# Kernel optimization log

Measured on AMD Instinct MI355X. Metric: run time of the kernel, lower is better.

Reference implementation:

```python
import jax, jax.numpy as jnp
import numpy as np

# --- obs layout constants (from source) ---
OBS_TERM_DIMS = (3, 3, 3, 3, 29, 29, 29, 96)
HISTORY_LEN = 5
BASE_LIN_VEL_DIM = 3
_OFFS = [0]
for d in OBS_TERM_DIMS[:-1]:
    _OFFS.append(_OFFS[-1] + d * HISTORY_LEN)

N = 131072

def _extract_frame(x, frame_idx):
    # proprio frame: 7 terms, 99 dims total
    parts = []
    for t in range(7):
        d = OBS_TERM_DIMS[t]
        s = _OFFS[t] + frame_idx * d
        parts.append(x[:, s:s + d])
    return jnp.concatenate(parts, axis=-1)

def _extract_elevation(x):
    s = _OFFS[7] + (HISTORY_LEN - 1) * OBS_TERM_DIMS[7]
    return x[:, s:s + OBS_TERM_DIMS[7]]  # [N,96]

def setup_inputs() -> dict:
    key = jax.random.key(0)
    ks = jax.random.split(key, 16)
    s = 0.05
    return {
        "x": jax.random.normal(ks[0], (N, 975), jnp.float32),
        "vae_W1": jax.random.normal(ks[1], (480, 256), jnp.float32) * s,
        "vae_b1": jnp.zeros((256,), jnp.float32),
        "vae_Wz": jax.random.normal(ks[2], (256, 32), jnp.float32) * s,
        "vae_bz": jnp.zeros((32,), jnp.float32),
        "vae_Wv": jax.random.normal(ks[3], (256, 3), jnp.float32) * s,
        "vae_bv": jnp.zeros((3,), jnp.float32),
        "ae_W1": jax.random.normal(ks[4], (96, 64), jnp.float32) * s,
        "ae_b1": jnp.zeros((64,), jnp.float32),
        "ae_W2": jax.random.normal(ks[5], (64, 32), jnp.float32) * s,
        "ae_b2": jnp.zeros((32,), jnp.float32),
        "gate_W1": jax.random.normal(ks[6], (32, 64), jnp.float32) * s,
        "gate_b1": jnp.zeros((64,), jnp.float32),
        "gate_W2": jax.random.normal(ks[7], (64, 5), jnp.float32) * s,
        "gate_b2": jnp.zeros((5,), jnp.float32),
        "eW1": jax.random.normal(ks[8], (5, 166, 128), jnp.float32) * s,
        "eb1": jnp.zeros((5, 128), jnp.float32),
        "eW2": jax.random.normal(ks[9], (5, 128, 128), jnp.float32) * s,
        "eb2": jnp.zeros((5, 128), jnp.float32),
        "eW3": jax.random.normal(ks[10], (5, 128, 29), jnp.float32) * s,
        "eb3": jnp.zeros((5, 29), jnp.float32),
    }

def reference(x, vae_W1, vae_b1, vae_Wz, vae_bz, vae_Wv, vae_bv,
              ae_W1, ae_b1, ae_W2, ae_b2,
              gate_W1, gate_b1, gate_W2, gate_b2,
              eW1, eb1, eW2, eb2, eW3, eb3):
    elu = jax.nn.elu
    # feature extraction
    o_t = _extract_frame(x, HISTORY_LEN - 1)                       # [N,99]
    frames = [_extract_frame(x, i)[:, BASE_LIN_VEL_DIM:] for i in range(HISTORY_LEN)]
    vae_hist = jnp.concatenate(frames, axis=-1)                    # [N,480]
    e_t = _extract_elevation(x)                                    # [N,96]
    # VAE estimator (no_grad in original)
    h = elu(vae_hist @ vae_W1 + vae_b1)
    z_H = jax.lax.stop_gradient(h @ vae_Wz + vae_bz)               # [N,32]
    v_pred = jax.lax.stop_gradient(h @ vae_Wv + vae_bv)            # [N,3]
    # AE estimator (no_grad)
    ha = elu(e_t @ ae_W1 + ae_b1)
    z_E = jax.lax.stop_gradient(ha @ ae_W2 + ae_b2)                # [N,32]
    # experts: batched GEMM over 5 experts
    inp = jnp.concatenate([o_t, v_pred, z_H, z_E], axis=-1)        # [N,166]
    h1 = elu(jnp.einsum('ni,eih->neh', inp, eW1) + eb1)            # [N,5,128]
    h2 = elu(jnp.einsum('neh,ehk->nek', h1, eW2) + eb2)            # [N,5,128]
    acts = jnp.einsum('neh,ehk->nek', h2, eW3) + eb3               # [N,5,29]
    # gating
    gl = elu(z_E @ gate_W1 + gate_b1) @ gate_W2 + gate_b2          # [N,5]
    w = jax.nn.softmax(gl, axis=-1)
    return jnp.einsum('ne,nek->nk', w, acts)                       # [N,29]
```

## Files before the change

kernel.cpp:

```cpp
#include <hip/hip_runtime.h>
#include <math.h>

typedef _Float16 f16;
typedef f16  f16x8 __attribute__((ext_vector_type(8)));
typedef float f32x4 __attribute__((ext_vector_type(4)));
typedef unsigned short ushort_t;

#define MFMA16(a, b, c) __builtin_amdgcn_mfma_f32_16x16x32_f16((a), (b), (c), 0, 0, 0)

#define W1T_E 0
#define WZV_E 131072
#define A1T_E 143360
#define A2T_E 149504
#define G1T_E 151552
#define G2T_E 153600
#define E1T_E 154624
#define E2T_E 277504
#define E3T_E 359424
#define F32_B 759808

#define S2_OFF   0
#define B0_OFF   36864
#define H2_OFF   17408
#define ELEV_OFF 62528
#define HA_OFF   62528
#define ZE_OFF   71744
#define WF_OFF   75840
#define SMEM_SZ  77888

__device__ __forceinline__ float elu_f(float v) {
    float e = __expf(v) - 1.f;
    return v > 0.f ? v : e;
}

__device__ __forceinline__ unsigned pk(float a, float b) {
    ushort_t u0 = __builtin_bit_cast(ushort_t, (f16)a);
    ushort_t u1 = __builtin_bit_cast(ushort_t, (f16)b);
    return (unsigned)u0 | ((unsigned)u1 << 16);
}

__device__ __forceinline__ void store4(f16* p, f32x4 v) {
    uint2 t; t.x = pk(v[0], v[1]); t.y = pk(v[2], v[3]);
    *(uint2*)p = t;
}

__device__ __forceinline__ void elu_store4(f16* p, f32x4 v) {
    uint2 t; t.x = pk(elu_f(v[0]), elu_f(v[1])); t.y = pk(elu_f(v[2]), elu_f(v[3]));
    *(uint2*)p = t;
}

__global__ void prep_kernel(const float* __restrict__ vW1, const float* __restrict__ vWz,
                            const float* __restrict__ vWv, const float* __restrict__ aW1,
                            const float* __restrict__ aW2, const float* __restrict__ gW1,
                            const float* __restrict__ gW2, const float* __restrict__ eW1,
                            const float* __restrict__ eW2, const float* __restrict__ eW3,
                            const float* __restrict__ vbz, const float* __restrict__ vbv,
                            const float* __restrict__ eb3, const float* __restrict__ gb2,
                            char* __restrict__ ws)
{
    int i = blockIdx.x * 256 + threadIdx.x;
    f16* H = (f16*)ws;
    if (i < 131072) {
        int c = i >> 9, ks = i & 511;
        int xcol = 12 + ks;
        float v = 0.f;
        if (xcol >= 15 && xcol <= 494) {
            int hc;
            if (xcol < 60) {
                int t = xcol / 15; int rm = xcol - 15 * t; int f = rm / 3;
                hc = 96 * f + 3 * (t - 1) + (rm - 3 * f);
            } else {
                int t2 = (xcol - 60) / 145; int rm = xcol - 60 - 145 * t2; int f = rm / 29;
                hc = 96 * f + 9 + 29 * t2 + (rm - 29 * f);
            }
            v = vW1[hc * 256 + c];
        }
        H[i] = (f16)v;
    } else if (i < 143360) {
        int j = i - 131072; int c = j / 256, k = j - c * 256;
        float v = (c < 32) ? vWz[k * 32 + c] : ((c < 35) ? vWv[k * 3 + (c - 32)] : 0.f);
        H[i] = (f16)v;
    } else if (i < 149504) {
        int j = i - 143360; int c = j / 96, k = j - c * 96;
        H[i] = (f16)aW1[k * 64 + c];
    } else if (i < 151552) {
        int j = i - 149504; int c = j / 64, k = j - c * 64;
        H[i] = (f16)aW2[k * 32 + c];
    } else if (i < 153600) {
        int j = i - 151552; int c = j / 32, k = j - c * 32;
        H[i] = (f16)gW1[k * 64 + c];
    } else if (i < 154624) {
        int j = i - 153600; int c = j / 64, k = j - c * 64;
        H[i] = (f16)((c < 5) ? gW2[k * 5 + c] : 0.f);
    } else if (i < 277504) {
        int j = i - 154624; int e = j / 24576, jj = j - e * 24576;
        int c = jj / 192, k = jj - c * 192;
        int ko = (k >= 5 && k < 107)   ? (k - 5)
               : (k >= 108 && k < 140) ? (k - 6)
               : (k >= 144 && k < 176) ? (k - 10) : -1;
        H[i] = (f16)((ko >= 0) ? eW1[(e * 166 + ko) * 128 + c] : 0.f);
    } else if (i < 359424) {
        int j = i - 277504; int e = j / 16384, jj = j - e * 16384;
        int c = jj / 128, k = jj - c * 128;
        H[i] = (f16)eW2[(e * 128 + k) * 128 + c];
    } else if (i < 379904) {
        int j = i - 359424; int e = j / 4096, jj = j - e * 4096;
        int c = jj / 128, k = jj - c * 128;
        H[i] = (f16)((c < 29) ? eW3[(e * 128 + k) * 29 + c] : 0.f);
    } else if (i < 380128) {
        int j = i - 379904;
        float* F = (float*)(ws + F32_B);
        float v;
        if (j < 48)       v = (j < 32) ? vbz[j] : ((j < 35) ? vbv[j - 32] : 0.f);
        else if (j < 208) { int t = j - 48; int e = t >> 5, c = t & 31;
                            v = (c < 29) ? eb3[e * 29 + c] : 0.f; }
        else              { int t = j - 208; v = (t < 5) ? gb2[t] : 0.f; }
        F[j] = v;
    }
}

__global__ __launch_bounds__(256, 2) void moe_fused(
    const float* __restrict__ x,
    const float* __restrict__ vb1,
    const float* __restrict__ ab1,
    const float* __restrict__ ab2,
    const float* __restrict__ gb1,
    const float* __restrict__ eb1,
    const float* __restrict__ eb2,
    const char* __restrict__ ws,
    float* __restrict__ out)
{
    __shared__ __align__(16) char smem[SMEM_SZ];
    const int tid  = threadIdx.x;
    const int wv   = tid >> 6;
    const int lane = tid & 63;
    const int lr   = lane & 15;
    const int lg   = lane >> 4;
    const int row0 = (int)blockIdx.x * 64;

    const f16* W1T = (const f16*)ws + W1T_E;
    const f16* WZV = (const f16*)ws + WZV_E;
    const f16* A1T = (const f16*)ws + A1T_E;
    const f16* A2T = (const f16*)ws + A2T_E;
    const f16* G1T = (const f16*)ws + G1T_E;
    const f16* G2T = (const f16*)ws + G2T_E;
    const f16* E1T = (const f16*)ws + E1T_E;
    const f16* E2T = (const f16*)ws + E2T_E;
    const f16* E3T = (const f16*)ws + E3T_E;
    const float* BZV  = (const float*)(ws + F32_B);
    const float* EB3P = BZV + 48;
    const float* GB2P = BZV + 208;

    f16* sS2 = (f16*)(smem + S2_OFF);
    f16* sEl = (f16*)(smem + ELEV_OFF);
    f16* sHA = (f16*)(smem + HA_OFF);
    f16* sZE = (f16*)(smem + ZE_OFF);
    f16* sH  = (f16*)(smem + S2_OFF);
    f16* sB0 = (f16*)(smem + B0_OFF);
    f16* sH1 = (f16*)(smem + S2_OFF);
    f16* sH2 = (f16*)(smem + H2_OFF);
    float* sWf = (float*)(smem + WF_OFF);

    {
        if (tid < 16) *(unsigned*)(smem + 62464 + 4 * tid) = 0u;
        const int sr0 = wv * 16;
        for (int rr = 0; rr < 16; ++rr) {
            const int r = sr0 + rr;
            const float* xr = x + (size_t)(row0 + r) * 975;
            if (lane < 48) {
                float a = xr[879 + 2 * lane], b = xr[880 + 2 * lane];
                *(unsigned*)(sEl + r * 104 + 2 * lane) = pk(a, b);
            }
            f16* dst = sS2 + r * 488;
#pragma unroll
            for (int j = 0; j < 4; ++j) {
                int p = j * 64 + lane;
                if (p < 244) {
                    float a = 0.f, b = 0.f;
                    if (p < 242) { a = xr[12 + 2 * p]; b = xr[13 + 2 * p]; }
                    *(unsigned*)(dst + 2 * p) = pk(a, b);
                }
            }
        }
    }
    __syncthreads();

    f32x4 g3acc[4];
    {
        f32x4 bi = *(const f32x4*)(ab1 + 16 * wv + 4 * lg);
#pragma unroll
        for (int m = 0; m < 4; ++m) g3acc[m] = bi;
#pragma unroll
        for (int ks = 0; ks < 3; ++ks) {
            f16x8 wf = *(const f16x8*)(A1T + (16 * wv + lr) * 96 + 32 * ks + 8 * lg);
#pragma unroll
            for (int m = 0; m < 4; ++m) {
                f16x8 bf = *(const f16x8*)(sEl + (16 * m + lr) * 104 + 32 * ks + 8 * lg);
                g3acc[m] = MFMA16(wf, bf, g3acc[m]);
            }
        }
    }
    __syncthreads();
#pragma unroll
    for (int m = 0; m < 4; ++m)
        elu_store4(sHA + (16 * m + lr) * 72 + 16 * wv + 4 * lg, g3acc[m]);
    __syncthreads();

    if (wv < 2) {
        f32x4 bi = *(const f32x4*)(ab2 + 16 * wv + 4 * lg);
        f32x4 acc[4];
#pragma unroll
        for (int m = 0; m < 4; ++m) acc[m] = bi;
#pragma unroll
        for (int ks = 0; ks < 2; ++ks) {
            f16x8 wf = *(const f16x8*)(A2T + (16 * wv + lr) * 64 + 32 * ks + 8 * lg);
#pragma unroll
            for (int m = 0; m < 4; ++m) {
                f16x8 bf = *(const f16x8*)(sHA + (16 * m + lr) * 72 + 32 * ks + 8 * lg);
                acc[m] = MFMA16(wf, bf, acc[m]);
            }
        }
#pragma unroll
        for (int m = 0; m < 4; ++m)
            store4(sZE + (16 * m + lr) * 32 + 16 * wv + 4 * lg, acc[m]);
    }
    __syncthreads();

    {
        f32x4 bi = *(const f32x4*)(gb1 + 16 * wv + 4 * lg);
        f32x4 acc[4];
#pragma unroll
        for (int m = 0; m < 4; ++m) acc[m] = bi;
        f16x8 wf = *(const f16x8*)(G1T + (16 * wv + lr) * 32 + 8 * lg);
#pragma unroll
        for (int m = 0; m < 4; ++m) {
            f16x8 bf = *(const f16x8*)(sZE + (16 * m + lr) * 32 + 8 * lg);
            acc[m] = MFMA16(wf, bf, acc[m]);
        }
#pragma unroll
        for (int m = 0; m < 4; ++m)
            elu_store4(sHA + (16 * m + lr) * 72 + 16 * wv + 4 * lg, acc[m]);
    }
    __syncthreads();

    if (wv == 0) {
        f32x4 bi = *(const f32x4*)(GB2P + 4 * lg);
        f32x4 acc[4];
#pragma unroll
        for (int m = 0; m < 4; ++m) acc[m] = bi;
#pragma unroll
        for (int ks = 0; ks < 2; ++ks) {
            f16x8 wf = *(const f16x8*)(G2T + lr * 64 + 32 * ks + 8 * lg);
#pragma unroll
            for (int m = 0; m < 4; ++m) {
                f16x8 bf = *(const f16x8*)(sHA + (16 * m + lr) * 72 + 32 * ks + 8 * lg);
                acc[m] = MFMA16(wf, bf, acc[m]);
            }
        }
        if (lg == 0) {
#pragma unroll
            for (int m = 0; m < 4; ++m)
                *(f32x4*)(sWf + (16 * m + lr) * 8) = acc[m];
        } else if (lg == 1) {
#pragma unroll
            for (int m = 0; m < 4; ++m)
                sWf[(16 * m + lr) * 8 + 4] = acc[m][0];
        }
    }
    __syncthreads();

    if (tid < 64) {
        float g[5];
#pragma unroll
        for (int e = 0; e < 5; ++e) g[e] = sWf[tid * 8 + e];
        float mx = fmaxf(fmaxf(fmaxf(g[0], g[1]), fmaxf(g[2], g[3])), g[4]);
        float s = 0.f;
#pragma unroll
        for (int e = 0; e < 5; ++e) { g[e] = __expf(g[e] - mx); s += g[e]; }
        float inv = 1.f / s;
#pragma unroll
        for (int e = 0; e < 5; ++e) sWf[tid * 8 + e] = g[e] * inv;
    }

    f32x4 acc1[4][4];
#pragma unroll
    for (int nt = 0; nt < 4; ++nt) {
        f32x4 bi = *(const f32x4*)(vb1 + 64 * wv + 16 * nt + 4 * lg);
#pragma unroll
        for (int m = 0; m < 4; ++m) acc1[m][nt] = bi;
    }
#pragma unroll
    for (int ks = 0; ks < 16; ++ks) {
        f16x8 wf[4];
#pragma unroll
        for (int nt = 0; nt < 4; ++nt)
            wf[nt] = *(const f16x8*)(W1T + (64 * wv + 16 * nt + lr) * 512 + 32 * ks + 8 * lg);
#pragma unroll
        for (int m = 0; m < 4; ++m) {
            f16x8 bf = *(const f16x8*)(sS2 + (16 * m + lr) * 488 + 32 * ks + 8 * lg);
#pragma unroll
            for (int nt = 0; nt < 4; ++nt)
                acc1[m][nt] = MFMA16(wf[nt], bf, acc1[m][nt]);
        }
    }
    const int r_ot = tid >> 2, sub = tid & 3;
    ushort_t otv[25];
#pragma unroll
    for (int i = 0; i < 25; ++i) {
        int j = sub + 4 * i;
        if (j < 99) {
            int s;
            if (j < 3) s = j;
            else if (j < 12) { int jj = j - 3; int t = jj / 3;
                               s = 15 * (t + 1) + (jj - 3 * t); }
            else { int jj = j - 12; int t2 = jj / 29;
                   s = 164 + 145 * t2 + (jj - 29 * t2); }
            otv[i] = __builtin_bit_cast(ushort_t, sS2[r_ot * 488 + s]);
        }
    }
    __syncthreads();

#pragma unroll
    for (int m = 0; m < 4; ++m)
#pragma unroll
        for (int nt = 0; nt < 4; ++nt)
            elu_store4(sH + (16 * m + lr) * 264 + 64 * wv + 16 * nt + 4 * lg, acc1[m][nt]);
#pragma unroll
    for (int i = 0; i < 25; ++i) {
        int j = sub + 4 * i;
        if (j < 99) sB0[r_ot * 200 + 5 + j] = __builtin_bit_cast(f16, otv[i]);
    }
    {
        char* b0r = (char*)sB0 + r_ot * 400;
        if (sub == 0) { *(uint2*)(b0r + 0) = (uint2){0u, 0u}; *(ushort_t*)(b0r + 8) = 0; }
        else if (sub == 1) { *(uint2*)(b0r + 280) = (uint2){0u, 0u}; }
        else if (sub == 2) { *(uint4*)(b0r + 352) = (uint4){0u,0u,0u,0u}; }
        else               { *(uint4*)(b0r + 368) = (uint4){0u,0u,0u,0u}; }
    }
#pragma unroll
    for (int it = 0; it < 2; ++it) {
        int idx = tid + 256 * it;
        int r = idx >> 3, c4 = idx & 7;
        uint2 v = *(uint2*)((char*)sZE + r * 64 + 8 * c4);
        *(uint2*)((char*)sB0 + r * 400 + 288 + 8 * c4) = v;
    }
    __syncthreads();

    if (wv < 3) {
        f32x4 bz = *(const f32x4*)(BZV + 16 * wv + 4 * lg);
        f32x4 acc[4];
#pragma unroll
        for (int m = 0; m < 4; ++m) acc[m] = bz;
#pragma unroll
        for (int ks = 0; ks < 8; ++ks) {
            f16x8 wf = *(const f16x8*)(WZV + (16 * wv + lr) * 256 + 32 * ks + 8 * lg);
#pragma unroll
            for (int m = 0; m < 4; ++m) {
                f16x8 bf = *(const f16x8*)(sH + (16 * m + lr) * 264 + 32 * ks + 8 * lg);
                acc[m] = MFMA16(wf, bf, acc[m]);
            }
        }
        int j0 = 16 * wv + 4 * lg;
        if (wv < 2 || lg == 0) {
            int col = (wv < 2) ? (108 + j0) : 104;
#pragma unroll
            for (int m = 0; m < 4; ++m)
                store4(sB0 + (16 * m + lr) * 200 + col, acc[m]);
        }
    }
    __syncthreads();

    f32x4 oacc[2];
    oacc[0] = (f32x4)0.f; oacc[1] = (f32x4)0.f;

    for (int e = 0; e < 5; ++e) {
        {
            f32x4 acc[4][2];
#pragma unroll
            for (int nt = 0; nt < 2; ++nt) {
                f32x4 bi = *(const f32x4*)(eb1 + e * 128 + 32 * wv + 16 * nt + 4 * lg);
#pragma unroll
                for (int m = 0; m < 4; ++m) acc[m][nt] = bi;
            }
#pragma unroll
            for (int ks = 0; ks < 6; ++ks) {
                f16x8 wf[2];
#pragma unroll
                for (int nt = 0; nt < 2; ++nt)
                    wf[nt] = *(const f16x8*)(E1T + (e * 128 + 32 * wv + 16 * nt + lr) * 192 + 32 * ks + 8 * lg);
#pragma unroll
                for (int m = 0; m < 4; ++m) {
                    f16x8 bf = *(const f16x8*)(sB0 + (16 * m + lr) * 200 + 32 * ks + 8 * lg);
#pragma unroll
                    for (int nt = 0; nt < 2; ++nt) acc[m][nt] = MFMA16(wf[nt], bf, acc[m][nt]);
                }
            }
#pragma unroll
            for (int m = 0; m < 4; ++m)
#pragma unroll
                for (int nt = 0; nt < 2; ++nt)
                    elu_store4(sH1 + (16 * m + lr) * 136 + 32 * wv + 16 * nt + 4 * lg, acc[m][nt]);
        }
        __syncthreads();
        {
            f32x4 acc[4][2];
#pragma unroll
            for (int nt = 0; nt < 2; ++nt) {
                f32x4 bi = *(const f32x4*)(eb2 + e * 128 + 32 * wv + 16 * nt + 4 * lg);
#pragma unroll
                for (int m = 0; m < 4; ++m) acc[m][nt] = bi;
            }
#pragma unroll
            for (int ks = 0; ks < 4; ++ks) {
                f16x8 wf[2];
#pragma unroll
                for (int nt = 0; nt < 2; ++nt)
                    wf[nt] = *(const f16x8*)(E2T + (e * 128 + 32 * wv + 16 * nt + lr) * 128 + 32 * ks + 8 * lg);
#pragma unroll
                for (int m = 0; m < 4; ++m) {
                    f16x8 bf = *(const f16x8*)(sH1 + (16 * m + lr) * 136 + 32 * ks + 8 * lg);
#pragma unroll
                    for (int nt = 0; nt < 2; ++nt) acc[m][nt] = MFMA16(wf[nt], bf, acc[m][nt]);
                }
            }
#pragma unroll
            for (int m = 0; m < 4; ++m)
#pragma unroll
                for (int nt = 0; nt < 2; ++nt)
                    elu_store4(sH2 + (16 * m + lr) * 136 + 32 * wv + 16 * nt + 4 * lg, acc[m][nt]);
        }
        __syncthreads();
        {
            f32x4 acc3[2];
#pragma unroll
            for (int nt = 0; nt < 2; ++nt)
                acc3[nt] = *(const f32x4*)(EB3P + e * 32 + 16 * nt + 4 * lg);
#pragma unroll
            for (int ks = 0; ks < 4; ++ks) {
                f16x8 bf = *(const f16x8*)(sH2 + (16 * wv + lr) * 136 + 32 * ks + 8 * lg);
#pragma unroll
                for (int nt = 0; nt < 2; ++nt) {
                    f16x8 wf = *(const f16x8*)(E3T + (e * 32 + 16 * nt + lr) * 128 + 32 * ks + 8 * lg);
                    acc3[nt] = MFMA16(wf, bf, acc3[nt]);
                }
            }
            float we = sWf[(16 * wv + lr) * 8 + e];
#pragma unroll
            for (int nt = 0; nt < 2; ++nt)
#pragma unroll
                for (int r = 0; r < 4; ++r) oacc[nt][r] += we * acc3[nt][r];
        }
        __syncthreads();
    }

    {
        int row = row0 + 16 * wv + lr;
#pragma unroll
        for (int nt = 0; nt < 2; ++nt)
#pragma unroll
            for (int r = 0; r < 4; ++r) {
                int col = 16 * nt + 4 * lg + r;
                if (col < 29) out[(size_t)row * 29 + col] = oacc[nt][r];
            }
    }
}

extern "C" void kernel_launch(void* const* d_in, const int* in_sizes, int n_in,
                              void* d_out, int out_size, void* d_ws, size_t ws_size,
                              hipStream_t stream)
{
    (void)n_in; (void)out_size; (void)ws_size;
    const float* x   = (const float*)d_in[0];
    const float* vW1 = (const float*)d_in[1];
    const float* vb1 = (const float*)d_in[2];
    const float* vWz = (const float*)d_in[3];
    const float* vbz = (const float*)d_in[4];
    const float* vWv = (const float*)d_in[5];
    const float* vbv = (const float*)d_in[6];
    const float* aW1 = (const float*)d_in[7];
    const float* ab1 = (const float*)d_in[8];
    const float* aW2 = (const float*)d_in[9];
    const float* ab2 = (const float*)d_in[10];
    const float* gW1 = (const float*)d_in[11];
    const float* gb1 = (const float*)d_in[12];
    const float* gW2 = (const float*)d_in[13];
    const float* gb2 = (const float*)d_in[14];
    const float* eW1 = (const float*)d_in[15];
    const float* eb1 = (const float*)d_in[16];
    const float* eW2 = (const float*)d_in[17];
    const float* eb2 = (const float*)d_in[18];
    const float* eW3 = (const float*)d_in[19];
    const float* eb3 = (const float*)d_in[20];

    int n = in_sizes[0] / 975;

    prep_kernel<<<(380128 + 255) / 256, 256, 0, stream>>>(
        vW1, vWz, vWv, aW1, aW2, gW1, gW2, eW1, eW2, eW3, vbz, vbv, eb3, gb2, (char*)d_ws);

    moe_fused<<<n / 64, 256, 0, stream>>>(
        x, vb1, ab1, ab2, gb1, eb1, eb2, (const char*)d_ws, (float*)d_out);
}
```

Measured before the change: 329.9 us.

## Prefetch weights across barriers and double-buffer W1 loads in fused MLP kernel

Global weight fragments for each stage are loaded into registers before the preceding barrier, and the VAE W1 loop is double-buffered so the next k-slice loads while the current one runs its MFMAs. The expert loop is fully unrolled, with the next expert's first-layer weights prefetched during the current expert's last layer. __syncthreads is replaced by a custom barrier that waits only on LDS counters, not on outstanding global loads, and MFMA sections are raised to higher wave priority. The aim is to hide global-memory latency behind compute and barriers, at the cost of much higher register pressure and possible occupancy loss.

```diff
diff --git a/kernel.cpp b/kernel.cpp
--- a/kernel.cpp
+++ b/kernel.cpp
@@ -47,6 +47,13 @@
 __device__ __forceinline__ void elu_store4(f16* p, f32x4 v) {
     uint2 t; t.x = pk(elu_f(v[0]), elu_f(v[1])); t.y = pk(elu_f(v[2]), elu_f(v[3]));
     *(uint2*)p = t;
+}
+
+__device__ __forceinline__ void sync_lds() {
+    asm volatile("s_waitcnt lgkmcnt(0)" ::: "memory");
+    __builtin_amdgcn_s_barrier();
+    asm volatile("" ::: "memory");
+    __builtin_amdgcn_sched_barrier(0);
 }
 
 __global__ void prep_kernel(const float* __restrict__ vW1, const float* __restrict__ vWz,
@@ -183,80 +190,89 @@
             }
         }
     }
-    __syncthreads();
+    f16x8 wg3[3]; f32x4 biG3 = *(const f32x4*)(ab1 + 16 * wv + 4 * lg);
+#pragma unroll
+    for (int ks = 0; ks < 3; ++ks)
+        wg3[ks] = *(const f16x8*)(A1T + (16 * wv + lr) * 96 + 32 * ks + 8 * lg);
+    sync_lds();
 
     f32x4 g3acc[4];
-    {
-        f32x4 bi = *(const f32x4*)(ab1 + 16 * wv + 4 * lg);
-#pragma unroll
-        for (int m = 0; m < 4; ++m) g3acc[m] = bi;
-#pragma unroll
-        for (int ks = 0; ks < 3; ++ks) {
-            f16x8 wf = *(const f16x8*)(A1T + (16 * wv + lr) * 96 + 32 * ks + 8 * lg);
-#pragma unroll
-            for (int m = 0; m < 4; ++m) {
-                f16x8 bf = *(const f16x8*)(sEl + (16 * m + lr) * 104 + 32 * ks + 8 * lg);
-                g3acc[m] = MFMA16(wf, bf, g3acc[m]);
-            }
-        }
-    }
-    __syncthreads();
+#pragma unroll
+    for (int m = 0; m < 4; ++m) g3acc[m] = biG3;
+    __builtin_amdgcn_s_setprio(1);
+#pragma unroll
+    for (int ks = 0; ks < 3; ++ks)
+#pragma unroll
+        for (int m = 0; m < 4; ++m) {
+            f16x8 bf = *(const f16x8*)(sEl + (16 * m + lr) * 104 + 32 * ks + 8 * lg);
+            g3acc[m] = MFMA16(wg3[ks], bf, g3acc[m]);
+        }
+    __builtin_amdgcn_s_setprio(0);
+    f16x8 wg4[2]; f32x4 biG4 = *(const f32x4*)(ab2 + 16 * wv + 4 * lg);
+#pragma unroll
+    for (int ks = 0; ks < 2; ++ks)
+        wg4[ks] = *(const f16x8*)(A2T + (16 * wv + lr) * 64 + 32 * ks + 8 * lg);
+    f16x8 wgh = *(const f16x8*)(G1T + (16 * wv + lr) * 32 + 8 * lg);
+    f32x4 biGH = *(const f32x4*)(gb1 + 16 * wv + 4 * lg);
+    sync_lds();
 #pragma unroll
     for (int m = 0; m < 4; ++m)
         elu_store4(sHA + (16 * m + lr) * 72 + 16 * wv + 4 * lg, g3acc[m]);
-    __syncthreads();
+    sync_lds();
 
     if (wv < 2) {
-        f32x4 bi = *(const f32x4*)(ab2 + 16 * wv + 4 * lg);
         f32x4 acc[4];
 #pragma unroll
-        for (int m = 0; m < 4; ++m) acc[m] = bi;
-#pragma unroll
-        for (int ks = 0; ks < 2; ++ks) {
-            f16x8 wf = *(const f16x8*)(A2T + (16 * wv + lr) * 64 + 32 * ks + 8 * lg);
+        for (int m = 0; m < 4; ++m) acc[m] = biG4;
+#pragma unroll
+        for (int ks = 0; ks < 2; ++ks)
 #pragma unroll
             for (int m = 0; m < 4; ++m) {
                 f16x8 bf = *(const f16x8*)(sHA + (16 * m + lr) * 72 + 32 * ks + 8 * lg);
-                acc[m] = MFMA16(wf, bf, acc[m]);
-            }
-        }
+                acc[m] = MFMA16(wg4[ks], bf, acc[m]);
+            }
 #pragma unroll
         for (int m = 0; m < 4; ++m)
             store4(sZE + (16 * m + lr) * 32 + 16 * wv + 4 * lg, acc[m]);
     }
-    __syncthreads();
+    f16x8 wgl[2]; f32x4 biGL = *(const f32x4*)(GB2P + 4 * lg);
+#pragma unroll
+    for (int ks = 0; ks < 2; ++ks)
+        wgl[ks] = *(const f16x8*)(G2T + lr * 64 + 32 * ks + 8 * lg);
+    sync_lds();
 
     {
-        f32x4 bi = *(const f32x4*)(gb1 + 16 * wv + 4 * lg);
         f32x4 acc[4];
 #pragma unroll
-        for (int m = 0; m < 4; ++m) acc[m] = bi;
-        f16x8 wf = *(const f16x8*)(G1T + (16 * wv + lr) * 32 + 8 * lg);
+        for (int m = 0; m < 4; ++m) acc[m] = biGH;
 #pragma unroll
         for (int m = 0; m < 4; ++m) {
             f16x8 bf = *(const f16x8*)(sZE + (16 * m + lr) * 32 + 8 * lg);
-            acc[m] = MFMA16(wf, bf, acc[m]);
+            acc[m] = MFMA16(wgh, bf, acc[m]);
         }
 #pragma unroll
         for (int m = 0; m < 4; ++m)
             elu_store4(sHA + (16 * m + lr) * 72 + 16 * wv + 4 * lg, acc[m]);
     }
-    __syncthreads();
+    f16x8 wq0[4]; f32x4 biG1[4];
+#pragma unroll
+    for (int nt = 0; nt < 4; ++nt) {
+        wq0[nt]  = *(const f16x8*)(W1T + (64 * wv + 16 * nt + lr) * 512 + 8 * lg);
+        biG1[nt] = *(const f32x4*)(vb1 + 64 * wv + 16 * nt + 4 * lg);
+    }
+    sync_lds();
 
     if (wv == 0) {
-        f32x4 bi = *(const f32x4*)(GB2P + 4 * lg);
         f32x4 acc[4];
 #pragma unroll
-        for (int m = 0; m < 4; ++m) acc[m] = bi;
-#pragma unroll
-        for (int ks = 0; ks < 2; ++ks) {
-            f16x8 wf = *(const f16x8*)(G2T + lr * 64 + 32 * ks + 8 * lg);
+        for (int m = 0; m < 4; ++m) acc[m] = biGL;
+#pragma unroll
+        for (int ks = 0; ks < 2; ++ks)
 #pragma unroll
             for (int m = 0; m < 4; ++m) {
                 f16x8 bf = *(const f16x8*)(sHA + (16 * m + lr) * 72 + 32 * ks + 8 * lg);
-                acc[m] = MFMA16(wf, bf, acc[m]);
-            }
-        }
+                acc[m] = MFMA16(wgl[ks], bf, acc[m]);
+            }
         if (lg == 0) {
 #pragma unroll
             for (int m = 0; m < 4; ++m)
@@ -267,7 +283,7 @@
                 sWf[(16 * m + lr) * 8 + 4] = acc[m][0];
         }
     }
-    __syncthreads();
+    sync_lds();
 
     if (tid < 64) {
         float g[5];
@@ -284,24 +300,39 @@
 
     f32x4 acc1[4][4];
 #pragma unroll
-    for (int nt = 0; nt < 4; ++nt) {
-        f32x4 bi = *(const f32x4*)(vb1 + 64 * wv + 16 * nt + 4 * lg);
-#pragma unroll
-        for (int m = 0; m < 4; ++m) acc1[m][nt] = bi;
-    }
-#pragma unroll
-    for (int ks = 0; ks < 16; ++ks) {
-        f16x8 wf[4];
-#pragma unroll
-        for (int nt = 0; nt < 4; ++nt)
-            wf[nt] = *(const f16x8*)(W1T + (64 * wv + 16 * nt + lr) * 512 + 32 * ks + 8 * lg);
-#pragma unroll
-        for (int m = 0; m < 4; ++m) {
-            f16x8 bf = *(const f16x8*)(sS2 + (16 * m + lr) * 488 + 32 * ks + 8 * lg);
+    for (int nt = 0; nt < 4; ++nt)
+#pragma unroll
+        for (int m = 0; m < 4; ++m) acc1[m][nt] = biG1[nt];
+    {
+        f16x8 wq1[4];
+        __builtin_amdgcn_s_setprio(1);
+#pragma unroll
+        for (int ks2 = 0; ks2 < 8; ++ks2) {
+            const int ksA = 2 * ks2, ksB = 2 * ks2 + 1;
 #pragma unroll
             for (int nt = 0; nt < 4; ++nt)
-                acc1[m][nt] = MFMA16(wf[nt], bf, acc1[m][nt]);
-        }
+                wq1[nt] = *(const f16x8*)(W1T + (64 * wv + 16 * nt + lr) * 512 + 32 * ksB + 8 * lg);
+#pragma unroll
+            for (int m = 0; m < 4; ++m) {
+                f16x8 bf = *(const f16x8*)(sS2 + (16 * m + lr) * 488 + 32 * ksA + 8 * lg);
+#pragma unroll
+                for (int nt = 0; nt < 4; ++nt)
+                    acc1[m][nt] = MFMA16(wq0[nt], bf, acc1[m][nt]);
+            }
+            if (ks2 < 7) {
+#pragma unroll
+                for (int nt = 0; nt < 4; ++nt)
+                    wq0[nt] = *(const f16x8*)(W1T + (64 * wv + 16 * nt + lr) * 512 + 32 * (ksA + 2) + 8 * lg);
+            }
+#pragma unroll
+            for (int m = 0; m < 4; ++m) {
+                f16x8 bf = *(const f16x8*)(sS2 + (16 * m + lr) * 488 + 32 * ksB + 8 * lg);
+#pragma unroll
+                for (int nt = 0; nt < 4; ++nt)
+                    acc1[m][nt] = MFMA16(wq1[nt], bf, acc1[m][nt]);
+            }
+        }
+        __builtin_amdgcn_s_setprio(0);
     }
     const int r_ot = tid >> 2, sub = tid & 3;
     ushort_t otv[25];
@@ -318,7 +349,14 @@
             otv[i] = __builtin_bit_cast(ushort_t, sS2[r_ot * 488 + s]);
         }
     }
-    __syncthreads();
+    f16x8 wzv[8]; f32x4 bzv;
+    if (wv < 3) {
+        bzv = *(const f32x4*)(BZV + 16 * wv + 4 * lg);
+#pragma unroll
+        for (int ks = 0; ks < 8; ++ks)
+            wzv[ks] = *(const f16x8*)(WZV + (16 * wv + lr) * 256 + 32 * ks + 8 * lg);
+    }
+    sync_lds();
 
 #pragma unroll
     for (int m = 0; m < 4; ++m)
@@ -344,22 +382,31 @@
         uint2 v = *(uint2*)((char*)sZE + r * 64 + 8 * c4);
         *(uint2*)((char*)sB0 + r * 400 + 288 + 8 * c4) = v;
     }
-    __syncthreads();
+    f16x8 wA[12]; f32x4 b1v[2];
+#pragma unroll
+    for (int ks = 0; ks < 6; ++ks)
+#pragma unroll
+        for (int nt = 0; nt < 2; ++nt)
+            wA[ks * 2 + nt] = *(const f16x8*)(E1T + (32 * wv + 16 * nt + lr) * 192 + 32 * ks + 8 * lg);
+#pragma unroll
+    for (int nt = 0; nt < 2; ++nt)
+        b1v[nt] = *(const f32x4*)(eb1 + 32 * wv + 16 * nt + 4 * lg);
+    float we5[5];
+#pragma unroll
+    for (int e = 0; e < 5; ++e) we5[e] = sWf[(16 * wv + lr) * 8 + e];
+    sync_lds();
 
     if (wv < 3) {
-        f32x4 bz = *(const f32x4*)(BZV + 16 * wv + 4 * lg);
         f32x4 acc[4];
 #pragma unroll
-        for (int m = 0; m < 4; ++m) acc[m] = bz;
-#pragma unroll
-        for (int ks = 0; ks < 8; ++ks) {
-            f16x8 wf = *(const f16x8*)(WZV + (16 * wv + lr) * 256 + 32 * ks + 8 * lg);
+        for (int m = 0; m < 4; ++m) acc[m] = bzv;
+#pragma unroll
+        for (int ks = 0; ks < 8; ++ks)
 #pragma unroll
             for (int m = 0; m < 4; ++m) {
                 f16x8 bf = *(const f16x8*)(sH + (16 * m + lr) * 264 + 32 * ks + 8 * lg);
-                acc[m] = MFMA16(wf, bf, acc[m]);
-            }
-        }
+                acc[m] = MFMA16(wzv[ks], bf, acc[m]);
+            }
         int j0 = 16 * wv + 4 * lg;
         if (wv < 2 || lg == 0) {
             int col = (wv < 2) ? (108 + j0) : 104;
@@ -368,100 +415,115 @@
                 store4(sB0 + (16 * m + lr) * 200 + col, acc[m]);
         }
     }
-    __syncthreads();
-
-    f32x4 oacc[2];
-    oacc[0] = (f32x4)0.f; oacc[1] = (f32x4)0.f;
-
+    sync_lds();
+
+    f32x4 oacc0 = (f32x4)0.f, oacc1 = (f32x4)0.f;
+#pragma unroll
     for (int e = 0; e < 5; ++e) {
         {
             f32x4 acc[4][2];
 #pragma unroll
-            for (int nt = 0; nt < 2; ++nt) {
-                f32x4 bi = *(const f32x4*)(eb1 + e * 128 + 32 * wv + 16 * nt + 4 * lg);
-#pragma unroll
-                for (int m = 0; m < 4; ++m) acc[m][nt] = bi;
-            }
-#pragma unroll
-            for (int ks = 0; ks < 6; ++ks) {
-                f16x8 wf[2];
-#pragma unroll
-                for (int nt = 0; nt < 2; ++nt)
-                    wf[nt] = *(const f16x8*)(E1T + (e * 128 + 32 * wv + 16 * nt + lr) * 192 + 32 * ks + 8 * lg);
+            for (int nt = 0; nt < 2; ++nt)
+#pragma unroll
+                for (int m = 0; m < 4; ++m) acc[m][nt] = b1v[nt];
+            __builtin_amdgcn_s_setprio(1);
+#pragma unroll
+            for (int ks = 0; ks < 6; ++ks)
 #pragma unroll
                 for (int m = 0; m < 4; ++m) {
                     f16x8 bf = *(const f16x8*)(sB0 + (16 * m + lr) * 200 + 32 * ks + 8 * lg);
 #pragma unroll
-                    for (int nt = 0; nt < 2; ++nt) acc[m][nt] = MFMA16(wf[nt], bf, acc[m][nt]);
+                    for (int nt = 0; nt < 2; ++nt)
+                        acc[m][nt] = MFMA16(wA[ks * 2 + nt], bf, acc[m][nt]);
                 }
-            }
+            __builtin_amdgcn_s_setprio(0);
+            f16x8 wB[8]; f32x4 b2v[2];
+#pragma unroll
+            for (int ks = 0; ks < 4; ++ks)
+#pragma unroll
+                for (int nt = 0; nt < 2; ++nt)
+                    wB[ks * 2 + nt] = *(const f16x8*)(E2T + (e * 128 + 32 * wv + 16 * nt + lr) * 128 + 32 * ks + 8 * lg);
+#pragma unroll
+            for (int nt = 0; nt < 2; ++nt)
+                b2v[nt] = *(const f32x4*)(eb2 + e * 128 + 32 * wv + 16 * nt + 4 * lg);
 #pragma unroll
             for (int m = 0; m < 4; ++m)
 #pragma unroll
                 for (int nt = 0; nt < 2; ++nt)
                     elu_store4(sH1 + (16 * m + lr) * 136 + 32 * wv + 16 * nt + 4 * lg, acc[m][nt]);
-        }
-        __syncthreads();
-        {
-            f32x4 acc[4][2];
-#pragma unroll
-            for (int nt = 0; nt < 2; ++nt) {
-                f32x4 bi = *(const f32x4*)(eb2 + e * 128 + 32 * wv + 16 * nt + 4 * lg);
-#pragma unroll
-                for (int m = 0; m < 4; ++m) acc[m][nt] = bi;
-            }
-#pragma unroll
-            for (int ks = 0; ks < 4; ++ks) {
-                f16x8 wf[2];
-#pragma unroll
-                for (int nt = 0; nt < 2; ++nt)
-                    wf[nt] = *(const f16x8*)(E2T + (e * 128 + 32 * wv + 16 * nt + lr) * 128 + 32 * ks + 8 * lg);
+            sync_lds();
+            f32x4 acc2[4][2];
+#pragma unroll
+            for (int nt = 0; nt < 2; ++nt)
+#pragma unroll
+                for (int m = 0; m < 4; ++m) acc2[m][nt] = b2v[nt];
+            __builtin_amdgcn_s_setprio(1);
+#pragma unroll
+            for (int ks = 0; ks < 4; ++ks)
 #pragma unroll
                 for (int m = 0; m < 4; ++m) {
                     f16x8 bf = *(const f16x8*)(sH1 + (16 * m + lr) * 136 + 32 * ks + 8 * lg);
 #pragma unroll
-                    for (int nt = 0; nt < 2; ++nt) acc[m][nt] = MFMA16(wf[nt], bf, acc[m][nt]);
+                    for (int nt = 0; nt < 2; ++nt)
+                        acc2[m][nt] = MFMA16(wB[ks * 2 + nt], bf, acc2[m][nt]);
                 }
-            }
+            __builtin_amdgcn_s_setprio(0);
+            f16x8 wC[8]; f32x4 b3v[2];
+#pragma unroll
+            for (int ks = 0; ks < 4; ++ks)
+#pragma unroll
+                for (int nt = 0; nt < 2; ++nt)
+                    wC[ks * 2 + nt] = *(const f16x8*)(E3T + (e * 32 + 16 * nt + lr) * 128 + 32 * ks + 8 * lg);
+#pragma unroll
+            for (int nt = 0; nt < 2; ++nt)
+                b3v[nt] = *(const f32x4*)(EB3P + e * 32 + 16 * nt + 4 * lg);
 #pragma unroll
             for (int m = 0; m < 4; ++m)
 #pragma unroll
                 for (int nt = 0; nt < 2; ++nt)
-                    elu_store4(sH2 + (16 * m + lr) * 136 + 32 * wv + 16 * nt + 4 * lg, acc[m][nt]);
-        }
-        __syncthreads();
-        {
-            f32x4 acc3[2];
-#pragma unroll
-            for (int nt = 0; nt < 2; ++nt)
-                acc3[nt] = *(const f32x4*)(EB3P + e * 32 + 16 * nt + 4 * lg);
+                    elu_store4(sH2 + (16 * m + lr) * 136 + 32 * wv + 16 * nt + 4 * lg, acc2[m][nt]);
+            sync_lds();
+            f32x4 a3[2];
+#pragma unroll
+            for (int nt = 0; nt < 2; ++nt) a3[nt] = b3v[nt];
+            __builtin_amdgcn_s_setprio(1);
 #pragma unroll
             for (int ks = 0; ks < 4; ++ks) {
                 f16x8 bf = *(const f16x8*)(sH2 + (16 * wv + lr) * 136 + 32 * ks + 8 * lg);
 #pragma unroll
-                for (int nt = 0; nt < 2; ++nt) {
-                    f16x8 wf = *(const f16x8*)(E3T + (e * 32 + 16 * nt + lr) * 128 + 32 * ks + 8 * lg);
-                    acc3[nt] = MFMA16(wf, bf, acc3[nt]);
-                }
-            }
-            float we = sWf[(16 * wv + lr) * 8 + e];
-#pragma unroll
-            for (int nt = 0; nt < 2; ++nt)
-#pragma unroll
-                for (int r = 0; r < 4; ++r) oacc[nt][r] += we * acc3[nt][r];
-        }
-        __syncthreads();
+                for (int nt = 0; nt < 2; ++nt)
+                    a3[nt] = MFMA16(wC[ks * 2 + nt], bf, a3[nt]);
+            }
+            __builtin_amdgcn_s_setprio(0);
+            if (e < 4) {
+#pragma unroll
+                for (int ks = 0; ks < 6; ++ks)
+#pragma unroll
+                    for (int nt = 0; nt < 2; ++nt)
+                        wA[ks * 2 + nt] = *(const f16x8*)(E1T + ((e + 1) * 128 + 32 * wv + 16 * nt + lr) * 192 + 32 * ks + 8 * lg);
+#pragma unroll
+                for (int nt = 0; nt < 2; ++nt)
+                    b1v[nt] = *(const f32x4*)(eb1 + (e + 1) * 128 + 32 * wv + 16 * nt + 4 * lg);
+            }
+            float we = we5[e];
+#pragma unroll
+            for (int r = 0; r < 4; ++r) {
+                oacc0[r] += we * a3[0][r];
+                oacc1[r] += we * a3[1][r];
+            }
+            sync_lds();
+        }
     }
 
     {
         int row = row0 + 16 * wv + lr;
 #pragma unroll
-        for (int nt = 0; nt < 2; ++nt)
-#pragma unroll
-            for (int r = 0; r < 4; ++r) {
-                int col = 16 * nt + 4 * lg + r;
-                if (col < 29) out[(size_t)row * 29 + col] = oacc[nt][r];
-            }
+        for (int r = 0; r < 4; ++r) {
+            int col0 = 4 * lg + r;
+            if (col0 < 29) out[(size_t)row * 29 + col0] = oacc0[r];
+            int col1 = 16 + 4 * lg + r;
+            if (col1 < 29) out[(size_t)row * 29 + col1] = oacc1[r];
+        }
     }
 }
 
```

Result: faster. 318.4 us (-3.5%).

## Double block to 512 threads, split per-wave MFMA work, lighter barriers

Applied to the files above, without the earlier changes.

The fused MoE kernel now runs 8 waves per 64-row block instead of 4, and every GEMM stage (AE, gating, VAE W1, expert layers) is split so each wave handles half the columns or rows. __syncthreads is replaced by a custom LDS-only wait plus s_barrier, and s_setprio is raised around the MFMA loops. Gating weights are read into registers early. The aim is more waves in flight per CU to hide latency and lower per-wave register pressure. The cost is fewer MFMAs per wave and the same number of barriers shared by more waves. Launch bounds of (512,4) may also force register spilling.

```diff
diff --git a/kernel.cpp b/kernel.cpp
--- a/kernel.cpp
+++ b/kernel.cpp
@@ -47,6 +47,13 @@
 __device__ __forceinline__ void elu_store4(f16* p, f32x4 v) {
     uint2 t; t.x = pk(elu_f(v[0]), elu_f(v[1])); t.y = pk(elu_f(v[2]), elu_f(v[3]));
     *(uint2*)p = t;
+}
+
+__device__ __forceinline__ void sync_lds() {
+    asm volatile("s_waitcnt lgkmcnt(0)" ::: "memory");
+    __builtin_amdgcn_s_barrier();
+    asm volatile("" ::: "memory");
+    __builtin_amdgcn_sched_barrier(0);
 }
 
 __global__ void prep_kernel(const float* __restrict__ vW1, const float* __restrict__ vWz,
@@ -119,7 +126,7 @@
     }
 }
 
-__global__ __launch_bounds__(256, 2) void moe_fused(
+__global__ __launch_bounds__(512, 4) void moe_fused(
     const float* __restrict__ x,
     const float* __restrict__ vb1,
     const float* __restrict__ ab1,
@@ -136,6 +143,8 @@
     const int lane = tid & 63;
     const int lr   = lane & 15;
     const int lg   = lane >> 4;
+    const int wh   = wv & 1;
+    const int wc   = wv >> 1;
     const int row0 = (int)blockIdx.x * 64;
 
     const f16* W1T = (const f16*)ws + W1T_E;
@@ -163,8 +172,8 @@
 
     {
         if (tid < 16) *(unsigned*)(smem + 62464 + 4 * tid) = 0u;
-        const int sr0 = wv * 16;
-        for (int rr = 0; rr < 16; ++rr) {
+        const int sr0 = wv * 8;
+        for (int rr = 0; rr < 8; ++rr) {
             const int r = sr0 + rr;
             const float* xr = x + (size_t)(row0 + r) * 975;
             if (lane < 48) {
@@ -183,80 +192,79 @@
             }
         }
     }
-    __syncthreads();
-
-    f32x4 g3acc[4];
-    {
-        f32x4 bi = *(const f32x4*)(ab1 + 16 * wv + 4 * lg);
-#pragma unroll
-        for (int m = 0; m < 4; ++m) g3acc[m] = bi;
+    sync_lds();
+
+    f32x4 g3acc[2];
+    {
+        f32x4 bi = *(const f32x4*)(ab1 + 16 * wc + 4 * lg);
+        g3acc[0] = bi; g3acc[1] = bi;
 #pragma unroll
         for (int ks = 0; ks < 3; ++ks) {
-            f16x8 wf = *(const f16x8*)(A1T + (16 * wv + lr) * 96 + 32 * ks + 8 * lg);
-#pragma unroll
-            for (int m = 0; m < 4; ++m) {
+            f16x8 wf = *(const f16x8*)(A1T + (16 * wc + lr) * 96 + 32 * ks + 8 * lg);
+#pragma unroll
+            for (int mm = 0; mm < 2; ++mm) {
+                int m = 2 * wh + mm;
                 f16x8 bf = *(const f16x8*)(sEl + (16 * m + lr) * 104 + 32 * ks + 8 * lg);
-                g3acc[m] = MFMA16(wf, bf, g3acc[m]);
-            }
-        }
-    }
-    __syncthreads();
-#pragma unroll
-    for (int m = 0; m < 4; ++m)
-        elu_store4(sHA + (16 * m + lr) * 72 + 16 * wv + 4 * lg, g3acc[m]);
-    __syncthreads();
-
-    if (wv < 2) {
-        f32x4 bi = *(const f32x4*)(ab2 + 16 * wv + 4 * lg);
+                g3acc[mm] = MFMA16(wf, bf, g3acc[mm]);
+            }
+        }
+    }
+    sync_lds();
+#pragma unroll
+    for (int mm = 0; mm < 2; ++mm)
+        elu_store4(sHA + (16 * (2 * wh + mm) + lr) * 72 + 16 * wc + 4 * lg, g3acc[mm]);
+    sync_lds();
+
+    if (wv < 4) {
+        int c = wv >> 1, h = wv & 1;
+        f32x4 bi = *(const f32x4*)(ab2 + 16 * c + 4 * lg);
+        f32x4 acc[2]; acc[0] = bi; acc[1] = bi;
+#pragma unroll
+        for (int ks = 0; ks < 2; ++ks) {
+            f16x8 wf = *(const f16x8*)(A2T + (16 * c + lr) * 64 + 32 * ks + 8 * lg);
+#pragma unroll
+            for (int mm = 0; mm < 2; ++mm) {
+                int m = 2 * h + mm;
+                f16x8 bf = *(const f16x8*)(sHA + (16 * m + lr) * 72 + 32 * ks + 8 * lg);
+                acc[mm] = MFMA16(wf, bf, acc[mm]);
+            }
+        }
+#pragma unroll
+        for (int mm = 0; mm < 2; ++mm)
+            store4(sZE + (16 * (2 * h + mm) + lr) * 32 + 16 * c + 4 * lg, acc[mm]);
+    }
+    sync_lds();
+
+    {
+        f32x4 bi = *(const f32x4*)(gb1 + 16 * wc + 4 * lg);
+        f32x4 acc[2]; acc[0] = bi; acc[1] = bi;
+        f16x8 wf = *(const f16x8*)(G1T + (16 * wc + lr) * 32 + 8 * lg);
+#pragma unroll
+        for (int mm = 0; mm < 2; ++mm) {
+            int m = 2 * wh + mm;
+            f16x8 bf = *(const f16x8*)(sZE + (16 * m + lr) * 32 + 8 * lg);
+            acc[mm] = MFMA16(wf, bf, acc[mm]);
+        }
+#pragma unroll
+        for (int mm = 0; mm < 2; ++mm)
+            elu_store4(sHA + (16 * (2 * wh + mm) + lr) * 72 + 16 * wc + 4 * lg, acc[mm]);
+    }
+    sync_lds();
+
+    if (wv == 0) {
+        f32x4 bi = *(const f32x4*)(GB2P + 4 * lg);
         f32x4 acc[4];
 #pragma unroll
         for (int m = 0; m < 4; ++m) acc[m] = bi;
 #pragma unroll
         for (int ks = 0; ks < 2; ++ks) {
-            f16x8 wf = *(const f16x8*)(A2T + (16 * wv + lr) * 64 + 32 * ks + 8 * lg);
+            f16x8 wf = *(const f16x8*)(G2T + lr * 64 + 32 * ks + 8 * lg);
 #pragma unroll
             for (int m = 0; m < 4; ++m) {
                 f16x8 bf = *(const f16x8*)(sHA + (16 * m + lr) * 72 + 32 * ks + 8 * lg);
                 acc[m] = MFMA16(wf, bf, acc[m]);
             }
         }
-#pragma unroll
-        for (int m = 0; m < 4; ++m)
-            store4(sZE + (16 * m + lr) * 32 + 16 * wv + 4 * lg, acc[m]);
-    }
-    __syncthreads();
-
-    {
-        f32x4 bi = *(const f32x4*)(gb1 + 16 * wv + 4 * lg);
-        f32x4 acc[4];
-#pragma unroll
-        for (int m = 0; m < 4; ++m) acc[m] = bi;
-        f16x8 wf = *(const f16x8*)(G1T + (16 * wv + lr) * 32 + 8 * lg);
-#pragma unroll
-        for (int m = 0; m < 4; ++m) {
-            f16x8 bf = *(const f16x8*)(sZE + (16 * m + lr) * 32 + 8 * lg);
-            acc[m] = MFMA16(wf, bf, acc[m]);
-        }
-#pragma unroll
-        for (int m = 0; m < 4; ++m)
-            elu_store4(sHA + (16 * m + lr) * 72 + 16 * wv + 4 * lg, acc[m]);
-    }
-    __syncthreads();
-
-    if (wv == 0) {
-        f32x4 bi = *(const f32x4*)(GB2P + 4 * lg);
-        f32x4 acc[4];
-#pragma unroll
-        for (int m = 0; m < 4; ++m) acc[m] = bi;
-#pragma unroll
-        for (int ks = 0; ks < 2; ++ks) {
-            f16x8 wf = *(const f16x8*)(G2T + lr * 64 + 32 * ks + 8 * lg);
-#pragma unroll
-            for (int m = 0; m < 4; ++m) {
-                f16x8 bf = *(const f16x8*)(sHA + (16 * m + lr) * 72 + 32 * ks + 8 * lg);
-                acc[m] = MFMA16(wf, bf, acc[m]);
-            }
-        }
         if (lg == 0) {
 #pragma unroll
             for (int m = 0; m < 4; ++m)
@@ -267,7 +275,7 @@
                 sWf[(16 * m + lr) * 8 + 4] = acc[m][0];
         }
     }
-    __syncthreads();
+    sync_lds();
 
     if (tid < 64) {
         float g[5];
@@ -282,32 +290,34 @@
         for (int e = 0; e < 5; ++e) sWf[tid * 8 + e] = g[e] * inv;
     }
 
-    f32x4 acc1[4][4];
-#pragma unroll
-    for (int nt = 0; nt < 4; ++nt) {
-        f32x4 bi = *(const f32x4*)(vb1 + 64 * wv + 16 * nt + 4 * lg);
+    f32x4 acc1[4][2];
+#pragma unroll
+    for (int nt = 0; nt < 2; ++nt) {
+        f32x4 bi = *(const f32x4*)(vb1 + 32 * wv + 16 * nt + 4 * lg);
 #pragma unroll
         for (int m = 0; m < 4; ++m) acc1[m][nt] = bi;
     }
+    __builtin_amdgcn_s_setprio(1);
 #pragma unroll
     for (int ks = 0; ks < 16; ++ks) {
-        f16x8 wf[4];
-#pragma unroll
-        for (int nt = 0; nt < 4; ++nt)
-            wf[nt] = *(const f16x8*)(W1T + (64 * wv + 16 * nt + lr) * 512 + 32 * ks + 8 * lg);
+        f16x8 wf[2];
+#pragma unroll
+        for (int nt = 0; nt < 2; ++nt)
+            wf[nt] = *(const f16x8*)(W1T + (32 * wv + 16 * nt + lr) * 512 + 32 * ks + 8 * lg);
 #pragma unroll
         for (int m = 0; m < 4; ++m) {
             f16x8 bf = *(const f16x8*)(sS2 + (16 * m + lr) * 488 + 32 * ks + 8 * lg);
 #pragma unroll
-            for (int nt = 0; nt < 4; ++nt)
+            for (int nt = 0; nt < 2; ++nt)
                 acc1[m][nt] = MFMA16(wf[nt], bf, acc1[m][nt]);
         }
     }
-    const int r_ot = tid >> 2, sub = tid & 3;
-    ushort_t otv[25];
-#pragma unroll
-    for (int i = 0; i < 25; ++i) {
-        int j = sub + 4 * i;
+    __builtin_amdgcn_s_setprio(0);
+    const int r_ot = tid >> 3, sub = tid & 7;
+    ushort_t otv[13];
+#pragma unroll
+    for (int i = 0; i < 13; ++i) {
+        int j = sub + 8 * i;
         if (j < 99) {
             int s;
             if (j < 3) s = j;
@@ -318,16 +328,17 @@
             otv[i] = __builtin_bit_cast(ushort_t, sS2[r_ot * 488 + s]);
         }
     }
-    __syncthreads();
+    float we5[5];
+    sync_lds();
 
 #pragma unroll
     for (int m = 0; m < 4; ++m)
 #pragma unroll
-        for (int nt = 0; nt < 4; ++nt)
-            elu_store4(sH + (16 * m + lr) * 264 + 64 * wv + 16 * nt + 4 * lg, acc1[m][nt]);
-#pragma unroll
-    for (int i = 0; i < 25; ++i) {
-        int j = sub + 4 * i;
+        for (int nt = 0; nt < 2; ++nt)
+            elu_store4(sH + (16 * m + lr) * 264 + 32 * wv + 16 * nt + 4 * lg, acc1[m][nt]);
+#pragma unroll
+    for (int i = 0; i < 13; ++i) {
+        int j = sub + 8 * i;
         if (j < 99) sB0[r_ot * 200 + 5 + j] = __builtin_bit_cast(f16, otv[i]);
     }
     {
@@ -335,133 +346,109 @@
         if (sub == 0) { *(uint2*)(b0r + 0) = (uint2){0u, 0u}; *(ushort_t*)(b0r + 8) = 0; }
         else if (sub == 1) { *(uint2*)(b0r + 280) = (uint2){0u, 0u}; }
         else if (sub == 2) { *(uint4*)(b0r + 352) = (uint4){0u,0u,0u,0u}; }
-        else               { *(uint4*)(b0r + 368) = (uint4){0u,0u,0u,0u}; }
-    }
-#pragma unroll
-    for (int it = 0; it < 2; ++it) {
-        int idx = tid + 256 * it;
-        int r = idx >> 3, c4 = idx & 7;
+        else if (sub == 3) { *(uint4*)(b0r + 368) = (uint4){0u,0u,0u,0u}; }
+    }
+    {
+        int r = tid >> 3, c4 = tid & 7;
         uint2 v = *(uint2*)((char*)sZE + r * 64 + 8 * c4);
         *(uint2*)((char*)sB0 + r * 400 + 288 + 8 * c4) = v;
     }
-    __syncthreads();
-
-    if (wv < 3) {
-        f32x4 bz = *(const f32x4*)(BZV + 16 * wv + 4 * lg);
-        f32x4 acc[4];
-#pragma unroll
-        for (int m = 0; m < 4; ++m) acc[m] = bz;
+#pragma unroll
+    for (int e = 0; e < 5; ++e) we5[e] = sWf[(16 * (wv & 3) + lr) * 8 + e];
+    sync_lds();
+
+    if (wv < 6) {
+        int c = wv >> 1, h = wv & 1;
+        f32x4 bz = *(const f32x4*)(BZV + 16 * c + 4 * lg);
+        f32x4 acc[2]; acc[0] = bz; acc[1] = bz;
 #pragma unroll
         for (int ks = 0; ks < 8; ++ks) {
-            f16x8 wf = *(const f16x8*)(WZV + (16 * wv + lr) * 256 + 32 * ks + 8 * lg);
-#pragma unroll
-            for (int m = 0; m < 4; ++m) {
+            f16x8 wf = *(const f16x8*)(WZV + (16 * c + lr) * 256 + 32 * ks + 8 * lg);
+#pragma unroll
+            for (int mm = 0; mm < 2; ++mm) {
+                int m = 2 * h + mm;
                 f16x8 bf = *(const f16x8*)(sH + (16 * m + lr) * 264 + 32 * ks + 8 * lg);
-                acc[m] = MFMA16(wf, bf, acc[m]);
-            }
-        }
-        int j0 = 16 * wv + 4 * lg;
-        if (wv < 2 || lg == 0) {
-            int col = (wv < 2) ? (108 + j0) : 104;
-#pragma unroll
-            for (int m = 0; m < 4; ++m)
-                store4(sB0 + (16 * m + lr) * 200 + col, acc[m]);
-        }
-    }
-    __syncthreads();
-
-    f32x4 oacc[2];
-    oacc[0] = (f32x4)0.f; oacc[1] = (f32x4)0.f;
+                acc[mm] = MFMA16(wf, bf, acc[mm]);
+            }
+        }
+        if (c < 2 || lg == 0) {
+            int col = (c < 2) ? (108 + 16 * c + 4 * lg) : 104;
+#pragma unroll
+            for (int mm = 0; mm < 2; ++mm)
+                store4(sB0 + (16 * (2 * h + mm) + lr) * 200 + col, acc[mm]);
+        }
+    }
+    sync_lds();
+
+    f32x4 oacc = (f32x4)0.f;
+    const int mrow = wv & 3;
+    const int nt3  = wv >> 2;
 
     for (int e = 0; e < 5; ++e) {
         {
-            f32x4 acc[4][2];
-#pragma unroll
-            for (int nt = 0; nt < 2; ++nt) {
-                f32x4 bi = *(const f32x4*)(eb1 + e * 128 + 32 * wv + 16 * nt + 4 * lg);
-#pragma unroll
-                for (int m = 0; m < 4; ++m) acc[m][nt] = bi;
-            }
+            f32x4 bi = *(const f32x4*)(eb1 + e * 128 + 16 * wv + 4 * lg);
+            f32x4 acc[4];
+#pragma unroll
+            for (int m = 0; m < 4; ++m) acc[m] = bi;
+            __builtin_amdgcn_s_setprio(1);
 #pragma unroll
             for (int ks = 0; ks < 6; ++ks) {
-                f16x8 wf[2];
-#pragma unroll
-                for (int nt = 0; nt < 2; ++nt)
-                    wf[nt] = *(const f16x8*)(E1T + (e * 128 + 32 * wv + 16 * nt + lr) * 192 + 32 * ks + 8 * lg);
+                f16x8 wf = *(const f16x8*)(E1T + (e * 128 + 16 * wv + lr) * 192 + 32 * ks + 8 * lg);
 #pragma unroll
                 for (int m = 0; m < 4; ++m) {
                     f16x8 bf = *(const f16x8*)(sB0 + (16 * m + lr) * 200 + 32 * ks + 8 * lg);
-#pragma unroll
-                    for (int nt = 0; nt < 2; ++nt) acc[m][nt] = MFMA16(wf[nt], bf, acc[m][nt]);
+                    acc[m] = MFMA16(wf, bf, acc[m]);
                 }
             }
+            __builtin_amdgcn_s_setprio(0);
 #pragma unroll
             for (int m = 0; m < 4; ++m)
-#pragma unroll
-                for (int nt = 0; nt < 2; ++nt)
-                    elu_store4(sH1 + (16 * m + lr) * 136 + 32 * wv + 16 * nt + 4 * lg, acc[m][nt]);
-        }
-        __syncthreads();
+                elu_store4(sH1 + (16 * m + lr) * 136 + 16 * wv + 4 * lg, acc[m]);
+        }
+        sync_lds();
         {
-            f32x4 acc[4][2];
-#pragma unroll
-            for (int nt = 0; nt < 2; ++nt) {
-                f32x4 bi = *(const f32x4*)(eb2 + e * 128 + 32 * wv + 16 * nt + 4 * lg);
-#pragma unroll
-                for (int m = 0; m < 4; ++m) acc[m][nt] = bi;
-            }
+            f32x4 bi = *(const f32x4*)(eb2 + e * 128 + 16 * wv + 4 * lg);
+            f32x4 acc[4];
+#pragma unroll
+            for (int m = 0; m < 4; ++m) acc[m] = bi;
+            __builtin_amdgcn_s_setprio(1);
 #pragma unroll
             for (int ks = 0; ks < 4; ++ks) {
-                f16x8 wf[2];
-#pragma unroll
-                for (int nt = 0; nt < 2; ++nt)
-                    wf[nt] = *(const f16x8*)(E2T + (e * 128 + 32 * wv + 16 * nt + lr) * 128 + 32 * ks + 8 * lg);
+                f16x8 wf = *(const f16x8*)(E2T + (e * 128 + 16 * wv + lr) * 128 + 32 * ks + 8 * lg);
 #pragma unroll
                 for (int m = 0; m < 4; ++m) {
                     f16x8 bf = *(const f16x8*)(sH1 + (16 * m + lr) * 136 + 32 * ks + 8 * lg);
-#pragma unroll
-                    for (int nt = 0; nt < 2; ++nt) acc[m][nt] = MFMA16(wf[nt], bf, acc[m][nt]);
+                    acc[m] = MFMA16(wf, bf, acc[m]);
                 }
             }
+            __builtin_amdgcn_s_setprio(0);
 #pragma unroll
             for (int m = 0; m < 4; ++m)
-#pragma unroll
-                for (int nt = 0; nt < 2; ++nt)
-                    elu_store4(sH2 + (16 * m + lr) * 136 + 32 * wv + 16 * nt + 4 * lg, acc[m][nt]);
-        }
-        __syncthreads();
+                elu_store4(sH2 + (16 * m + lr) * 136 + 16 * wv + 4 * lg, acc[m]);
+        }
+        sync_lds();
         {
-            f32x4 acc3[2];
-#pragma unroll
-            for (int nt = 0; nt < 2; ++nt)
-                acc3[nt] = *(const f32x4*)(EB3P + e * 32 + 16 * nt + 4 * lg);
+            f32x4 a3 = *(const f32x4*)(EB3P + e * 32 + 16 * nt3 + 4 * lg);
 #pragma unroll
             for (int ks = 0; ks < 4; ++ks) {
-                f16x8 bf = *(const f16x8*)(sH2 + (16 * wv + lr) * 136 + 32 * ks + 8 * lg);
-#pragma unroll
-                for (int nt = 0; nt < 2; ++nt) {
-                    f16x8 wf = *(const f16x8*)(E3T + (e * 32 + 16 * nt + lr) * 128 + 32 * ks + 8 * lg);
-                    acc3[nt] = MFMA16(wf, bf, acc3[nt]);
-                }
-            }
-            float we = sWf[(16 * wv + lr) * 8 + e];
-#pragma unroll
-            for (int nt = 0; nt < 2; ++nt)
-#pragma unroll
-                for (int r = 0; r < 4; ++r) oacc[nt][r] += we * acc3[nt][r];
-        }
-        __syncthreads();
-    }
-
-    {
-        int row = row0 + 16 * wv + lr;
-#pragma unroll
-        for (int nt = 0; nt < 2; ++nt)
-#pragma unroll
-            for (int r = 0; r < 4; ++r) {
-                int col = 16 * nt + 4 * lg + r;
-                if (col < 29) out[(size_t)row * 29 + col] = oacc[nt][r];
-            }
+                f16x8 bf = *(const f16x8*)(sH2 + (16 * mrow + lr) * 136 + 32 * ks + 8 * lg);
+                f16x8 wf = *(const f16x8*)(E3T + (e * 32 + 16 * nt3 + lr) * 128 + 32 * ks + 8 * lg);
+                a3 = MFMA16(wf, bf, a3);
+            }
+            float we = we5[e];
+#pragma unroll
+            for (int r = 0; r < 4; ++r) oacc[r] += we * a3[r];
+        }
+        sync_lds();
+    }
+
+    {
+        int row = row0 + 16 * mrow + lr;
+#pragma unroll
+        for (int r = 0; r < 4; ++r) {
+            int col = 16 * nt3 + 4 * lg + r;
+            if (col < 29) out[(size_t)row * 29 + col] = oacc[r];
+        }
     }
 }
 
@@ -497,6 +484,6 @@
     prep_kernel<<<(380128 + 255) / 256, 256, 0, stream>>>(
         vW1, vWz, vWv, aW1, aW2, gW1, gW2, eW1, eW2, eW3, vbz, vbv, eb3, gb2, (char*)d_ws);
 
-    moe_fused<<<n / 64, 256, 0, stream>>>(
+    moe_fused<<<n / 64, 512, 0, stream>>>(
         x, vb1, ab1, ab2, gb1, eb1, eb2, (const char*)d_ws, (float*)d_out);
 }
```

After: 298.7 us. -9.5%, faster.
